# Performance work log

Measured on AMD Instinct MI355X. Metric: run time of the kernel, lower is better.

## Reference

```python
import jax, jax.numpy as jnp
import numpy as np

CD_W1 = 1.0
CD_W2 = 1.0


def setup_inputs() -> dict:
    key = jax.random.key(0)
    k1, k2 = jax.random.split(key)
    B, N, M, D = 16, 4096, 4096, 3
    points1 = jax.random.normal(k1, (B, N, D), dtype=jnp.float32)
    points2 = jax.random.normal(k2, (B, M, D), dtype=jnp.float32)
    return {"points1": points1, "points2": points2}


def reference(points1, points2):
    # squared pairwise distances via |a|^2 + |b|^2 - 2 a.b (GEMM form)
    a2 = jnp.sum(points1 * points1, axis=-1)          # [B, N]
    b2 = jnp.sum(points2 * points2, axis=-1)          # [B, M]
    ab = jnp.einsum("bnd,bmd->bnm", points1, points2)  # [B, N, M]
    dist = a2[:, :, None] + b2[:, None, :] - 2.0 * ab   # [B, N, M]
    dist_min1 = jnp.min(dist, axis=2)                  # nearest in points2 for each point1
    dist_min2 = jnp.min(dist, axis=1)                  # nearest in points1 for each point2
    B = points1.shape[0]
    return (CD_W1 * jnp.sum(dist_min1) + CD_W2 * jnp.sum(dist_min2)) / B
```

## Files before the change

### kernel.cpp

```cpp
#include <hip/hip_runtime.h>

#define BQ     16
#define NPTS   4096
#define TOTAL  (BQ * NPTS)
#define NPART  128

#define ROWMIN_FLOATS ((size_t)8 * TOTAL)
#define WS_NEED (ROWMIN_FLOATS * 4 + (size_t)NPART * 4)

typedef __attribute__((ext_vector_type(8))) short short8;
typedef __attribute__((ext_vector_type(4))) float f32x4;

__device__ __forceinline__ unsigned short f2bf(float x) {
    union { float f; unsigned u; } v; v.f = x;
    unsigned r = v.u + 0x7FFFu + ((v.u >> 16) & 1u);
    return (unsigned short)(r >> 16);
}
__device__ __forceinline__ float bf2f(unsigned short h) {
    union { float f; unsigned u; } v; v.u = ((unsigned)h) << 16; return v.f;
}
#define BF_ONE 0x3F80

__device__ __forceinline__ uint4 make_bslots16(const float* __restrict__ pts,
                                               int tile, int lane32) {
    const int g = lane32 >> 4;
    const float* pp = pts + (size_t)(tile * 16 + (lane32 & 15)) * 3;
    const float x = pp[0], y = pp[1], z = pp[2];
    const unsigned short xh = f2bf(x), yh = f2bf(y), zh = f2bf(z);
    const unsigned short xl = f2bf(x - bf2f(xh)), yl = f2bf(y - bf2f(yh)),
                         zl = f2bf(z - bf2f(zh));
    const unsigned short m2xh = f2bf(-2.0f * bf2f(xh)), m2yh = f2bf(-2.0f * bf2f(yh)),
                         m2zh = f2bf(-2.0f * bf2f(zh));
    const unsigned short m2xl = f2bf(-2.0f * bf2f(xl)), m2yl = f2bf(-2.0f * bf2f(yl)),
                         m2zl = f2bf(-2.0f * bf2f(zl));
    const float s2 = fmaf(x, x, fmaf(y, y, z * z));
    const unsigned short s2h = f2bf(s2);
    const unsigned short s2l = f2bf(s2 - bf2f(s2h));
    unsigned short s[8];
    if (g == 0) { s[0]=m2xh; s[1]=m2yh; s[2]=m2zh; s[3]=m2xl;   s[4]=m2yl;   s[5]=m2zl; s[6]=m2xh; s[7]=m2yh; }
    else        { s[0]=m2zh; s[1]=BF_ONE; s[2]=BF_ONE; s[3]=s2h; s[4]=s2l;   s[5]=0;    s[6]=0;    s[7]=0;    }
    uint4 o;
    o.x = (unsigned)s[0] | ((unsigned)s[1] << 16);
    o.y = (unsigned)s[2] | ((unsigned)s[3] << 16);
    o.z = (unsigned)s[4] | ((unsigned)s[5] << 16);
    o.w = (unsigned)s[6] | ((unsigned)s[7] << 16);
    return o;
}

__device__ __forceinline__ short8 make_aslots16(const float* __restrict__ pts,
                                                int point, int g) {
    const float* pp = pts + (size_t)point * 3;
    const float x = pp[0], y = pp[1], z = pp[2];
    const unsigned short xh = f2bf(x), yh = f2bf(y), zh = f2bf(z);
    const unsigned short xl = f2bf(x - bf2f(xh)), yl = f2bf(y - bf2f(yh)),
                         zl = f2bf(z - bf2f(zh));
    const float s2 = fmaf(x, x, fmaf(y, y, z * z));
    const unsigned short s2h = f2bf(s2);
    const unsigned short s2l = f2bf(s2 - bf2f(s2h));
    unsigned short s[8];
    if (g == 0) { s[0]=xh; s[1]=yh; s[2]=zh; s[3]=xh;     s[4]=yh;     s[5]=zh; s[6]=xl; s[7]=yl; }
    else        { s[0]=zl; s[1]=s2h; s[2]=s2l; s[3]=BF_ONE; s[4]=BF_ONE; s[5]=0; s[6]=0; s[7]=0; }
    union { unsigned u[4]; short8 v; } o;
    o.u[0] = (unsigned)s[0] | ((unsigned)s[1] << 16);
    o.u[1] = (unsigned)s[2] | ((unsigned)s[3] << 16);
    o.u[2] = (unsigned)s[4] | ((unsigned)s[5] << 16);
    o.u[3] = (unsigned)s[6] | ((unsigned)s[7] << 16);
    return o.v;
}

__global__ __launch_bounds__(256, 4) void cd_main(
        const float* __restrict__ p1, const float* __restrict__ p2,
        float* __restrict__ rowmin) {
    const int dir  = blockIdx.y;
    const float* __restrict__ A  = dir ? p2 : p1;
    const float* __restrict__ Bp = dir ? p1 : p2;

    const int bx   = blockIdx.x;
    const int b    = bx >> 5;
    const int rg   = (bx >> 2) & 7;
    const int cg   = bx & 3;
    const int wave = threadIdx.x >> 6;
    const int lane = threadIdx.x & 63;
    const int half = lane >> 5;

    __shared__ uint4 spanel[64 * 32];

    const float* __restrict__ Bbase = Bp + (size_t)(b * NPTS + cg * 1024) * 3;
#pragma unroll
    for (int k = 0; k < 8; ++k) {
        const int s = threadIdx.x + k * 256;
        spanel[s] = make_bslots16(Bbase, s >> 5, s & 31);
    }

    const int rowbase = b * NPTS + rg * 512 + wave * 128;

    short8 az; { union { unsigned u[4]; short8 v; } z = {{0,0,0,0}}; az = z.v; }
    short8 a0=az,a1=az,a2=az,a3=az,a4=az,a5=az,a6=az,a7=az;
    if (half == 0) {
        const int g = (lane >> 4) & 1, r = lane & 15;
        a0 = make_aslots16(A, rowbase +   0 + r, g);
        a1 = make_aslots16(A, rowbase +  16 + r, g);
        a2 = make_aslots16(A, rowbase +  32 + r, g);
        a3 = make_aslots16(A, rowbase +  48 + r, g);
        a4 = make_aslots16(A, rowbase +  64 + r, g);
        a5 = make_aslots16(A, rowbase +  80 + r, g);
        a6 = make_aslots16(A, rowbase +  96 + r, g);
        a7 = make_aslots16(A, rowbase + 112 + r, g);
    }

    f32x4 zero = {0.0f, 0.0f, 0.0f, 0.0f};
    f32x4 r0,r1,r2,r3,r4,r5,r6,r7;
#pragma unroll
    for (int e = 0; e < 4; ++e) {
        r0[e]=3.0e38f; r1[e]=3.0e38f; r2[e]=3.0e38f; r3[e]=3.0e38f;
        r4[e]=3.0e38f; r5[e]=3.0e38f; r6[e]=3.0e38f; r7[e]=3.0e38f;
    }

    __syncthreads();

#define CD_COMPUTE(C0, C1)                                                   \
    do {                                                                     \
        const short8 bf0 = *reinterpret_cast<const short8*>(&(C0));          \
        const short8 bf1 = *reinterpret_cast<const short8*>(&(C1));          \
        f32x4 d0, d1;                                                        \
        d0 = __builtin_amdgcn_mfma_f32_16x16x32_bf16(a0, bf0, zero, 0,0,0);  \
        d1 = __builtin_amdgcn_mfma_f32_16x16x32_bf16(a0, bf1, zero, 0,0,0);  \
        _Pragma("unroll") for (int e = 0; e < 4; ++e)                        \
            r0[e] = fminf(r0[e], fminf(d0[e], d1[e]));                       \
        d0 = __builtin_amdgcn_mfma_f32_16x16x32_bf16(a1, bf0, zero, 0,0,0);  \
        d1 = __builtin_amdgcn_mfma_f32_16x16x32_bf16(a1, bf1, zero, 0,0,0);  \
        _Pragma("unroll") for (int e = 0; e < 4; ++e)                        \
            r1[e] = fminf(r1[e], fminf(d0[e], d1[e]));                       \
        d0 = __builtin_amdgcn_mfma_f32_16x16x32_bf16(a2, bf0, zero, 0,0,0);  \
        d1 = __builtin_amdgcn_mfma_f32_16x16x32_bf16(a2, bf1, zero, 0,0,0);  \
        _Pragma("unroll") for (int e = 0; e < 4; ++e)                        \
            r2[e] = fminf(r2[e], fminf(d0[e], d1[e]));                       \
        d0 = __builtin_amdgcn_mfma_f32_16x16x32_bf16(a3, bf0, zero, 0,0,0);  \
        d1 = __builtin_amdgcn_mfma_f32_16x16x32_bf16(a3, bf1, zero, 0,0,0);  \
        _Pragma("unroll") for (int e = 0; e < 4; ++e)                        \
            r3[e] = fminf(r3[e], fminf(d0[e], d1[e]));                       \
        d0 = __builtin_amdgcn_mfma_f32_16x16x32_bf16(a4, bf0, zero, 0,0,0);  \
        d1 = __builtin_amdgcn_mfma_f32_16x16x32_bf16(a4, bf1, zero, 0,0,0);  \
        _Pragma("unroll") for (int e = 0; e < 4; ++e)                        \
            r4[e] = fminf(r4[e], fminf(d0[e], d1[e]));                       \
        d0 = __builtin_amdgcn_mfma_f32_16x16x32_bf16(a5, bf0, zero, 0,0,0);  \
        d1 = __builtin_amdgcn_mfma_f32_16x16x32_bf16(a5, bf1, zero, 0,0,0);  \
        _Pragma("unroll") for (int e = 0; e < 4; ++e)                        \
            r5[e] = fminf(r5[e], fminf(d0[e], d1[e]));                       \
        d0 = __builtin_amdgcn_mfma_f32_16x16x32_bf16(a6, bf0, zero, 0,0,0);  \
        d1 = __builtin_amdgcn_mfma_f32_16x16x32_bf16(a6, bf1, zero, 0,0,0);  \
        _Pragma("unroll") for (int e = 0; e < 4; ++e)                        \
            r6[e] = fminf(r6[e], fminf(d0[e], d1[e]));                       \
        d0 = __builtin_amdgcn_mfma_f32_16x16x32_bf16(a7, bf0, zero, 0,0,0);  \
        d1 = __builtin_amdgcn_mfma_f32_16x16x32_bf16(a7, bf1, zero, 0,0,0);  \
        _Pragma("unroll") for (int e = 0; e < 4; ++e)                        \
            r7[e] = fminf(r7[e], fminf(d0[e], d1[e]));                       \
    } while (0)

    const int sl = lane & 31;
    int idx = wave * 16;
    uint4 c0 = spanel[idx * 32 + sl], c1 = spanel[(idx + 1) * 32 + sl];
#pragma unroll 1
    for (int i = 0; i < 31; ++i) {
        const int nidx = (idx + 2) & 63;
        uint4 n0 = spanel[nidx * 32 + sl];
        uint4 n1 = spanel[(nidx + 1) * 32 + sl];
        CD_COMPUTE(c0, c1);
        c0 = n0; c1 = n1; idx = nidx;
    }
    CD_COMPUTE(c0, c1);
#undef CD_COMPUTE

    float* __restrict__ outr = rowmin + (size_t)(dir * 4 + cg) * TOTAL;
    const int rgrp = lane >> 4;
#pragma unroll
    for (int s = 0; s < 8; ++s) {
        f32x4 rv = (s==0)?r0:(s==1)?r1:(s==2)?r2:(s==3)?r3:(s==4)?r4:(s==5)?r5:(s==6)?r6:r7;
#pragma unroll
        for (int e = 0; e < 4; ++e) {
            float v = rv[e];
            v = fminf(v, __shfl_xor(v, 1));
            v = fminf(v, __shfl_xor(v, 2));
            v = fminf(v, __shfl_xor(v, 4));
            v = fminf(v, __shfl_xor(v, 8));
            if ((lane & 15) == 0)
                outr[rowbase + s * 16 + rgrp * 4 + e] = fmaxf(v, 0.0f);
        }
    }
}

__global__ __launch_bounds__(256) void cd_combine(const float* __restrict__ rowmin,
                                                  float* __restrict__ partial) {
    __shared__ float sred[256];
    const int tid = blockIdx.x * 256 + threadIdx.x;
    float s = 0.0f;
#pragma unroll
    for (int k = 0; k < 4; ++k) {
        const int i   = tid + k * 32768;
        const int d   = i >> 16;
        const int row = i & (TOTAL - 1);
        const float* base = rowmin + (size_t)d * 4 * TOTAL + row;
        s += fminf(fminf(base[0], base[TOTAL]),
                   fminf(base[2 * TOTAL], base[3 * TOTAL]));
    }
    sred[threadIdx.x] = s;
    __syncthreads();
    for (int st = 128; st > 0; st >>= 1) {
        if (threadIdx.x < st) sred[threadIdx.x] += sred[threadIdx.x + st];
        __syncthreads();
    }
    if (threadIdx.x == 0) partial[blockIdx.x] = sred[0];
}

__global__ __launch_bounds__(NPART) void cd_final(const float* __restrict__ partial,
                                                  float* __restrict__ out) {
    __shared__ float sred[NPART];
    sred[threadIdx.x] = partial[threadIdx.x];
    __syncthreads();
    for (int st = NPART / 2; st > 0; st >>= 1) {
        if (threadIdx.x < st) sred[threadIdx.x] += sred[threadIdx.x + st];
        __syncthreads();
    }
    if (threadIdx.x == 0) out[0] = sred[0] * (1.0f / (float)BQ);
}

__global__ __launch_bounds__(256) void cd_init_ws(unsigned int* __restrict__ ws) {
    ws[blockIdx.x * 256 + threadIdx.x] = 0x7F800000u;
}
#define F_APT 8
__global__ __launch_bounds__(256) void cd_min_lds(
        const float* __restrict__ p1, const float* __restrict__ p2,
        unsigned int* __restrict__ wsmin) {
    const int dir = blockIdx.y;
    const float* __restrict__ Aset = dir ? p2 : p1;
    const float* __restrict__ Bset = dir ? p1 : p2;
    unsigned int* __restrict__ outmin = wsmin + dir * TOTAL;
    const int atile = blockIdx.x / 16;
    const int mtile = blockIdx.x % 16;
    const int a0 = atile * 2048;
    const int m0 = (a0 / NPTS) * NPTS + mtile * 256;
    __shared__ float4 sbf[256];
    {
        const float* bpn = Bset + (size_t)(m0 + threadIdx.x) * 3;
        float bx = bpn[0], by = bpn[1], bz = bpn[2];
        sbf[threadIdx.x] = make_float4(-2.0f*bx, -2.0f*by, -2.0f*bz,
                                       fmaf(bx,bx,fmaf(by,by,bz*bz)));
    }
    __syncthreads();
    float ax[F_APT], ay[F_APT], az_[F_APT], q2[F_APT], mn[F_APT];
#pragma unroll
    for (int k = 0; k < F_APT; ++k) {
        const int ai = a0 + k*256 + threadIdx.x;
        const float* ap = Aset + (size_t)ai * 3;
        ax[k]=ap[0]; ay[k]=ap[1]; az_[k]=ap[2];
        q2[k]=fmaf(ax[k],ax[k],fmaf(ay[k],ay[k],az_[k]*az_[k]));
        mn[k]=3.0e38f;
    }
#pragma unroll 2
    for (int j = 0; j < 256; j += 2) {
        const float4 b0 = sbf[j], b1 = sbf[j+1];
#pragma unroll
        for (int k = 0; k < F_APT; ++k) {
            float d0 = fmaf(az_[k],b0.z,b0.w); d0=fmaf(ay[k],b0.y,d0); d0=fmaf(ax[k],b0.x,d0);
            float d1 = fmaf(az_[k],b1.z,b1.w); d1=fmaf(ay[k],b1.y,d1); d1=fmaf(ax[k],b1.x,d1);
            mn[k] = fminf(fminf(mn[k], d0), d1);
        }
    }
#pragma unroll
    for (int k = 0; k < F_APT; ++k) {
        const int ai = a0 + k*256 + threadIdx.x;
        atomicMin(&outmin[ai], __float_as_uint(fmaxf(q2[k]+mn[k], 0.0f)));
    }
}
__global__ __launch_bounds__(1024) void cd_reduce_single(const float* __restrict__ wsmin,
                                                         float* __restrict__ out) {
    __shared__ float sred[1024];
    const float4* __restrict__ v = (const float4*)wsmin;
    float s = 0.0f;
    for (int i = threadIdx.x; i < (2*TOTAL)/4; i += 1024) {
        float4 x = v[i]; s += (x.x + x.y) + (x.z + x.w);
    }
    sred[threadIdx.x] = s;
    __syncthreads();
    for (int st = 512; st > 0; st >>= 1) {
        if (threadIdx.x < st) sred[threadIdx.x] += sred[threadIdx.x + st];
        __syncthreads();
    }
    if (threadIdx.x == 0) out[0] = sred[0] * (1.0f / (float)BQ);
}

extern "C" void kernel_launch(void* const* d_in, const int* in_sizes, int n_in,
                              void* d_out, int out_size, void* d_ws, size_t ws_size,
                              hipStream_t stream) {
    const float* p1 = (const float*)d_in[0];
    const float* p2 = (const float*)d_in[1];
    float* out = (float*)d_out;

    if (ws_size >= WS_NEED) {
        float* rowmin  = (float*)d_ws;
        float* partial = (float*)((char*)d_ws + ROWMIN_FLOATS * 4);

        dim3 grid(512, 2, 1);
        cd_main<<<grid, 256, 0, stream>>>(p1, p2, rowmin);
        cd_combine<<<128, 256, 0, stream>>>(rowmin, partial);
        cd_final<<<1, NPART, 0, stream>>>(partial, out);
    } else {
        unsigned* wsmin = (unsigned*)d_ws;
        cd_init_ws<<<(2 * TOTAL) / 256, 256, 0, stream>>>(wsmin);
        dim3 grid(512, 2, 1);
        cd_min_lds<<<grid, 256, 0, stream>>>(p1, p2, wsmin);
        cd_reduce_single<<<1, 1024, 0, stream>>>((const float*)wsmin, out);
    }
}
```

Before: 41.96 us.

## Switch distance MFMA from 16x16x32 to 32x32x16 tiles with full-lane A usage

Replaces the 16x16x32 bf16 MFMA tiling with 32x32x16 bf16 MFMAs so that all 64 lanes hold useful A data, instead of half the lanes being zero-padded. The earlier K=32 tiles wasted half the reduction depth on zeros; K=16 matches the 16 bf16 slots of the split-precision encoding. Each wave now covers 64 rows instead of 128, so the grid doubles to 1024 blocks and the B panel is re-laid out as 32-point tiles. The row-min reduction now shuffles across 32 lanes with a different row mapping, which adds risk in the output indexing.

Result: faster. 40.58 us (-3.3%).

```diff
diff --git a/kernel.cpp b/kernel.cpp
--- a/kernel.cpp
+++ b/kernel.cpp
@@ -8,8 +8,8 @@
 #define ROWMIN_FLOATS ((size_t)8 * TOTAL)
 #define WS_NEED (ROWMIN_FLOATS * 4 + (size_t)NPART * 4)
 
-typedef __attribute__((ext_vector_type(8))) short short8;
-typedef __attribute__((ext_vector_type(4))) float f32x4;
+typedef __attribute__((ext_vector_type(8)))  short short8;
+typedef __attribute__((ext_vector_type(16))) float f32x16;
 
 __device__ __forceinline__ unsigned short f2bf(float x) {
     union { float f; unsigned u; } v; v.f = x;
@@ -21,10 +21,10 @@
 }
 #define BF_ONE 0x3F80
 
-__device__ __forceinline__ uint4 make_bslots16(const float* __restrict__ pts,
-                                               int tile, int lane32) {
-    const int g = lane32 >> 4;
-    const float* pp = pts + (size_t)(tile * 16 + (lane32 & 15)) * 3;
+__device__ __forceinline__ uint4 make_bslots(const float* __restrict__ pts,
+                                             int tile, int lane) {
+    const int pidx = lane & 31, g = lane >> 5;
+    const float* pp = pts + (size_t)(tile * 32 + pidx) * 3;
     const float x = pp[0], y = pp[1], z = pp[2];
     const unsigned short xh = f2bf(x), yh = f2bf(y), zh = f2bf(z);
     const unsigned short xl = f2bf(x - bf2f(xh)), yl = f2bf(y - bf2f(yh)),
@@ -37,8 +37,8 @@
     const unsigned short s2h = f2bf(s2);
     const unsigned short s2l = f2bf(s2 - bf2f(s2h));
     unsigned short s[8];
-    if (g == 0) { s[0]=m2xh; s[1]=m2yh; s[2]=m2zh; s[3]=m2xl;   s[4]=m2yl;   s[5]=m2zl; s[6]=m2xh; s[7]=m2yh; }
-    else        { s[0]=m2zh; s[1]=BF_ONE; s[2]=BF_ONE; s[3]=s2h; s[4]=s2l;   s[5]=0;    s[6]=0;    s[7]=0;    }
+    if (g == 0) { s[0]=m2xh; s[1]=m2yh; s[2]=m2zh; s[3]=m2xl; s[4]=m2yl; s[5]=m2zl; s[6]=m2xh; s[7]=m2yh; }
+    else        { s[0]=m2zh; s[1]=BF_ONE; s[2]=BF_ONE; s[3]=s2h; s[4]=s2l; s[5]=0; s[6]=0; s[7]=0; }
     uint4 o;
     o.x = (unsigned)s[0] | ((unsigned)s[1] << 16);
     o.y = (unsigned)s[2] | ((unsigned)s[3] << 16);
@@ -47,8 +47,8 @@
     return o;
 }
 
-__device__ __forceinline__ short8 make_aslots16(const float* __restrict__ pts,
-                                                int point, int g) {
+__device__ __forceinline__ short8 make_aslots(const float* __restrict__ pts,
+                                              int point, int g) {
     const float* pp = pts + (size_t)point * 3;
     const float x = pp[0], y = pp[1], z = pp[2];
     const unsigned short xh = f2bf(x), yh = f2bf(y), zh = f2bf(z);
@@ -58,7 +58,7 @@
     const unsigned short s2h = f2bf(s2);
     const unsigned short s2l = f2bf(s2 - bf2f(s2h));
     unsigned short s[8];
-    if (g == 0) { s[0]=xh; s[1]=yh; s[2]=zh; s[3]=xh;     s[4]=yh;     s[5]=zh; s[6]=xl; s[7]=yl; }
+    if (g == 0) { s[0]=xh; s[1]=yh; s[2]=zh; s[3]=xh; s[4]=yh; s[5]=zh; s[6]=xl; s[7]=yl; }
     else        { s[0]=zl; s[1]=s2h; s[2]=s2l; s[3]=BF_ONE; s[4]=BF_ONE; s[5]=0; s[6]=0; s[7]=0; }
     union { unsigned u[4]; short8 v; } o;
     o.u[0] = (unsigned)s[0] | ((unsigned)s[1] << 16);
@@ -76,115 +76,74 @@
     const float* __restrict__ Bp = dir ? p1 : p2;
 
     const int bx   = blockIdx.x;
-    const int b    = bx >> 5;
-    const int rg   = (bx >> 2) & 7;
+    const int b    = bx >> 6;
+    const int rg   = (bx >> 2) & 15;
     const int cg   = bx & 3;
     const int wave = threadIdx.x >> 6;
     const int lane = threadIdx.x & 63;
-    const int half = lane >> 5;
-
-    __shared__ uint4 spanel[64 * 32];
+    const int pidx = lane & 31, g = lane >> 5;
+
+    __shared__ uint4 spanel[32 * 64];
 
     const float* __restrict__ Bbase = Bp + (size_t)(b * NPTS + cg * 1024) * 3;
 #pragma unroll
     for (int k = 0; k < 8; ++k) {
         const int s = threadIdx.x + k * 256;
-        spanel[s] = make_bslots16(Bbase, s >> 5, s & 31);
-    }
-
-    const int rowbase = b * NPTS + rg * 512 + wave * 128;
-
-    short8 az; { union { unsigned u[4]; short8 v; } z = {{0,0,0,0}}; az = z.v; }
-    short8 a0=az,a1=az,a2=az,a3=az,a4=az,a5=az,a6=az,a7=az;
-    if (half == 0) {
-        const int g = (lane >> 4) & 1, r = lane & 15;
-        a0 = make_aslots16(A, rowbase +   0 + r, g);
-        a1 = make_aslots16(A, rowbase +  16 + r, g);
-        a2 = make_aslots16(A, rowbase +  32 + r, g);
-        a3 = make_aslots16(A, rowbase +  48 + r, g);
-        a4 = make_aslots16(A, rowbase +  64 + r, g);
-        a5 = make_aslots16(A, rowbase +  80 + r, g);
-        a6 = make_aslots16(A, rowbase +  96 + r, g);
-        a7 = make_aslots16(A, rowbase + 112 + r, g);
-    }
-
-    f32x4 zero = {0.0f, 0.0f, 0.0f, 0.0f};
-    f32x4 r0,r1,r2,r3,r4,r5,r6,r7;
-#pragma unroll
-    for (int e = 0; e < 4; ++e) {
-        r0[e]=3.0e38f; r1[e]=3.0e38f; r2[e]=3.0e38f; r3[e]=3.0e38f;
-        r4[e]=3.0e38f; r5[e]=3.0e38f; r6[e]=3.0e38f; r7[e]=3.0e38f;
-    }
-
-    __syncthreads();
-
-#define CD_COMPUTE(C0, C1)                                                   \
-    do {                                                                     \
-        const short8 bf0 = *reinterpret_cast<const short8*>(&(C0));          \
-        const short8 bf1 = *reinterpret_cast<const short8*>(&(C1));          \
-        f32x4 d0, d1;                                                        \
-        d0 = __builtin_amdgcn_mfma_f32_16x16x32_bf16(a0, bf0, zero, 0,0,0);  \
-        d1 = __builtin_amdgcn_mfma_f32_16x16x32_bf16(a0, bf1, zero, 0,0,0);  \
-        _Pragma("unroll") for (int e = 0; e < 4; ++e)                        \
-            r0[e] = fminf(r0[e], fminf(d0[e], d1[e]));                       \
-        d0 = __builtin_amdgcn_mfma_f32_16x16x32_bf16(a1, bf0, zero, 0,0,0);  \
-        d1 = __builtin_amdgcn_mfma_f32_16x16x32_bf16(a1, bf1, zero, 0,0,0);  \
-        _Pragma("unroll") for (int e = 0; e < 4; ++e)                        \
-            r1[e] = fminf(r1[e], fminf(d0[e], d1[e]));                       \
-        d0 = __builtin_amdgcn_mfma_f32_16x16x32_bf16(a2, bf0, zero, 0,0,0);  \
-        d1 = __builtin_amdgcn_mfma_f32_16x16x32_bf16(a2, bf1, zero, 0,0,0);  \
-        _Pragma("unroll") for (int e = 0; e < 4; ++e)                        \
-            r2[e] = fminf(r2[e], fminf(d0[e], d1[e]));                       \
-        d0 = __builtin_amdgcn_mfma_f32_16x16x32_bf16(a3, bf0, zero, 0,0,0);  \
-        d1 = __builtin_amdgcn_mfma_f32_16x16x32_bf16(a3, bf1, zero, 0,0,0);  \
-        _Pragma("unroll") for (int e = 0; e < 4; ++e)                        \
-            r3[e] = fminf(r3[e], fminf(d0[e], d1[e]));                       \
-        d0 = __builtin_amdgcn_mfma_f32_16x16x32_bf16(a4, bf0, zero, 0,0,0);  \
-        d1 = __builtin_amdgcn_mfma_f32_16x16x32_bf16(a4, bf1, zero, 0,0,0);  \
-        _Pragma("unroll") for (int e = 0; e < 4; ++e)                        \
-            r4[e] = fminf(r4[e], fminf(d0[e], d1[e]));                       \
-        d0 = __builtin_amdgcn_mfma_f32_16x16x32_bf16(a5, bf0, zero, 0,0,0);  \
-        d1 = __builtin_amdgcn_mfma_f32_16x16x32_bf16(a5, bf1, zero, 0,0,0);  \
-        _Pragma("unroll") for (int e = 0; e < 4; ++e)                        \
-            r5[e] = fminf(r5[e], fminf(d0[e], d1[e]));                       \
-        d0 = __builtin_amdgcn_mfma_f32_16x16x32_bf16(a6, bf0, zero, 0,0,0);  \
-        d1 = __builtin_amdgcn_mfma_f32_16x16x32_bf16(a6, bf1, zero, 0,0,0);  \
-        _Pragma("unroll") for (int e = 0; e < 4; ++e)                        \
-            r6[e] = fminf(r6[e], fminf(d0[e], d1[e]));                       \
-        d0 = __builtin_amdgcn_mfma_f32_16x16x32_bf16(a7, bf0, zero, 0,0,0);  \
-        d1 = __builtin_amdgcn_mfma_f32_16x16x32_bf16(a7, bf1, zero, 0,0,0);  \
-        _Pragma("unroll") for (int e = 0; e < 4; ++e)                        \
-            r7[e] = fminf(r7[e], fminf(d0[e], d1[e]));                       \
+        spanel[s] = make_bslots(Bbase, s >> 6, s & 63);
+    }
+
+    const int rowbase = b * NPTS + rg * 256 + wave * 64;
+
+    const short8 a0 = make_aslots(A, rowbase      + pidx, g);
+    const short8 a1 = make_aslots(A, rowbase + 32 + pidx, g);
+
+    f32x16 zero, r0, r1;
+#pragma unroll
+    for (int e = 0; e < 16; ++e) { zero[e] = 0.0f; r0[e] = 3.0e38f; r1[e] = 3.0e38f; }
+
+    __syncthreads();
+
+#define CD_COMPUTE(C0, C1)                                                    \
+    do {                                                                      \
+        const short8 bf0 = *reinterpret_cast<const short8*>(&(C0));           \
+        const short8 bf1 = *reinterpret_cast<const short8*>(&(C1));           \
+        f32x16 d0, d1;                                                        \
+        d0 = __builtin_amdgcn_mfma_f32_32x32x16_bf16(a0, bf0, zero, 0, 0, 0); \
+        d1 = __builtin_amdgcn_mfma_f32_32x32x16_bf16(a0, bf1, zero, 0, 0, 0); \
+        _Pragma("unroll") for (int e = 0; e < 16; ++e)                        \
+            r0[e] = fminf(r0[e], fminf(d0[e], d1[e]));                        \
+        d0 = __builtin_amdgcn_mfma_f32_32x32x16_bf16(a1, bf0, zero, 0, 0, 0); \
+        d1 = __builtin_amdgcn_mfma_f32_32x32x16_bf16(a1, bf1, zero, 0, 0, 0); \
+        _Pragma("unroll") for (int e = 0; e < 16; ++e)                        \
+            r1[e] = fminf(r1[e], fminf(d0[e], d1[e]));                        \
     } while (0)
 
-    const int sl = lane & 31;
-    int idx = wave * 16;
-    uint4 c0 = spanel[idx * 32 + sl], c1 = spanel[(idx + 1) * 32 + sl];
+    int t0 = wave * 8;
+    uint4 c0 = spanel[t0 * 64 + lane], c1 = spanel[(t0 + 1) * 64 + lane];
 #pragma unroll 1
-    for (int i = 0; i < 31; ++i) {
-        const int nidx = (idx + 2) & 63;
-        uint4 n0 = spanel[nidx * 32 + sl];
-        uint4 n1 = spanel[(nidx + 1) * 32 + sl];
+    for (int i = 0; i < 15; ++i) {
+        const int tn = (t0 + 2) & 31;
+        uint4 n0 = spanel[tn * 64 + lane];
+        uint4 n1 = spanel[(tn + 1) * 64 + lane];
         CD_COMPUTE(c0, c1);
-        c0 = n0; c1 = n1; idx = nidx;
+        c0 = n0; c1 = n1; t0 = tn;
     }
     CD_COMPUTE(c0, c1);
 #undef CD_COMPUTE
 
     float* __restrict__ outr = rowmin + (size_t)(dir * 4 + cg) * TOTAL;
-    const int rgrp = lane >> 4;
-#pragma unroll
-    for (int s = 0; s < 8; ++s) {
-        f32x4 rv = (s==0)?r0:(s==1)?r1:(s==2)?r2:(s==3)?r3:(s==4)?r4:(s==5)?r5:(s==6)?r6:r7;
-#pragma unroll
-        for (int e = 0; e < 4; ++e) {
-            float v = rv[e];
-            v = fminf(v, __shfl_xor(v, 1));
-            v = fminf(v, __shfl_xor(v, 2));
-            v = fminf(v, __shfl_xor(v, 4));
-            v = fminf(v, __shfl_xor(v, 8));
-            if ((lane & 15) == 0)
-                outr[rowbase + s * 16 + rgrp * 4 + e] = fmaxf(v, 0.0f);
+#pragma unroll
+    for (int e = 0; e < 16; ++e) {
+        float v0 = r0[e], v1 = r1[e];
+#pragma unroll
+        for (int m = 1; m <= 16; m <<= 1) {
+            v0 = fminf(v0, __shfl_xor(v0, m));
+            v1 = fminf(v1, __shfl_xor(v1, m));
+        }
+        const int rl = (e & 3) + 8 * (e >> 2) + 4 * g;
+        if (pidx == 0) {
+            outr[rowbase +      rl] = fmaxf(v0, 0.0f);
+            outr[rowbase + 32 + rl] = fmaxf(v1, 0.0f);
         }
     }
 }
@@ -300,7 +259,7 @@
         float* rowmin  = (float*)d_ws;
         float* partial = (float*)((char*)d_ws + ROWMIN_FLOATS * 4);
 
-        dim3 grid(512, 2, 1);
+        dim3 grid(1024, 2, 1);
         cd_main<<<grid, 256, 0, stream>>>(p1, p2, rowmin);
         cd_combine<<<128, 256, 0, stream>>>(rowmin, partial);
         cd_final<<<1, NPART, 0, stream>>>(partial, out);
```
